# Kernel tuning notes

Hardware: AMD Instinct MI355X
Metric: run time of the kernel (lower is better)

The kernel has to match this reference:

```python
import jax, jax.numpy as jnp
import numpy as np

N_NODES = 100000
N_EDGES = 1600000
IN_FEATURES = 128
OUT_FEATURES = 32


def setup_inputs() -> dict:
    key = jax.random.key(0)
    k_x, k_w, k_r, k_c, k_v = jax.random.split(key, 5)
    x = jax.random.normal(k_x, (N_NODES, IN_FEATURES), dtype=jnp.float32)
    # One fused (in_features, out_features) weight == concat of the out_features Dense(in,1) layers
    W = jax.random.normal(k_w, (IN_FEATURES, OUT_FEATURES), dtype=jnp.float32) / np.sqrt(IN_FEATURES)
    b = jnp.zeros((OUT_FEATURES,), dtype=jnp.float32)
    edge_rows = jax.random.randint(k_r, (N_EDGES,), 0, N_NODES, dtype=jnp.int64)
    edge_cols = jax.random.randint(k_c, (N_EDGES,), 0, N_NODES, dtype=jnp.int64)
    edge_vals = jax.random.uniform(k_v, (N_EDGES,), dtype=jnp.float32)
    return {"x": x, "W": W, "b": b, "edge_rows": edge_rows,
            "edge_cols": edge_cols, "edge_vals": edge_vals}


def reference(x, W, b, edge_rows, edge_cols, edge_vals):
    # z_i = dense_i(x) for all i at once: (N, out_features)
    z = x @ W + b
    # per nonzero edge e=(r,c) with adjacency value w_e:
    #   (z*adj).values + (z^T*adj).values = w_e * (z[r] + z[c])   -> (E, out_features)
    out = edge_vals[:, None] * (z[edge_rows] + z[edge_cols])
    return out
```

## Files before the change

kernel.cpp:

```cpp
#include <hip/hip_runtime.h>

#define NODES 100000
#define IN_F 128
#define OUT_F 32

__global__ __launch_bounds__(256) void zgemm_kernel(
    const float* __restrict__ x, const float* __restrict__ W,
    const float* __restrict__ b, float* __restrict__ z, int n_nodes)
{
    __shared__ float xs[64 * IN_F];
    __shared__ float Ws[IN_F * OUT_F];
    __shared__ float bs[OUT_F];

    const int t = threadIdx.x;
    const int row0 = blockIdx.x * 64;
    const int rows = min(64, n_nodes - row0);

    {
        const float4* Wv = (const float4*)W;
        float4* Wsv = (float4*)Ws;
        #pragma unroll
        for (int i = 0; i < 4; ++i)
            Wsv[t + i * 256] = Wv[t + i * 256];
        if (t < OUT_F) bs[t] = b[t];
    }
    {
        const float4* xv = (const float4*)(x + (size_t)row0 * IN_F);
        float4* xsv = (float4*)xs;
        const int nv = rows * (IN_F / 4);
        for (int i = t; i < nv; i += 256)
            xsv[i] = xv[i];
    }
    __syncthreads();

    const int col = t & 31;
    const int rg  = t >> 5;

    float acc[8];
    #pragma unroll
    for (int i = 0; i < 8; ++i) acc[i] = 0.f;

    for (int k = 0; k < IN_F; ++k) {
        const float wv = Ws[k * OUT_F + col];
        #pragma unroll
        for (int i = 0; i < 8; ++i)
            acc[i] += xs[(rg + i * 8) * IN_F + k] * wv;
    }

    const float bb = bs[col];
    #pragma unroll
    for (int i = 0; i < 8; ++i) {
        const int r = rg + i * 8;
        if (r < rows)
            z[(size_t)(row0 + r) * OUT_F + col] = acc[i] + bb;
    }
}

__global__ __launch_bounds__(256) void edge_kernel(
    const int* __restrict__ erows, const int* __restrict__ ecols,
    const float* __restrict__ evals, const float* __restrict__ z,
    float* __restrict__ out, int n_edges)
{
    const size_t g = (size_t)blockIdx.x * 256 + threadIdx.x;
    const size_t e = g >> 3;
    if (e >= (size_t)n_edges) return;
    const int joff = (int)(g & 7) << 2;

    const int r = erows[e];
    const int c = ecols[e];
    const float w = evals[e];

    const float4 zr = *(const float4*)(z + (size_t)r * OUT_F + joff);
    const float4 zc = *(const float4*)(z + (size_t)c * OUT_F + joff);

    float4 o;
    o.x = w * (zr.x + zc.x);
    o.y = w * (zr.y + zc.y);
    o.z = w * (zr.z + zc.z);
    o.w = w * (zr.w + zc.w);

    *(float4*)(out + e * OUT_F + joff) = o;
}

extern "C" void kernel_launch(void* const* d_in, const int* in_sizes, int n_in,
                              void* d_out, int out_size, void* d_ws, size_t ws_size,
                              hipStream_t stream)
{
    const float* x  = (const float*)d_in[0];
    const float* W  = (const float*)d_in[1];
    const float* b  = (const float*)d_in[2];
    const int* erow = (const int*)d_in[3];
    const int* ecol = (const int*)d_in[4];
    const float* ev = (const float*)d_in[5];

    const int n_nodes = in_sizes[0] / IN_F;
    const int n_edges = in_sizes[3];

    float* z   = (float*)d_ws;
    float* out = (float*)d_out;

    const int gemm_blocks = (n_nodes + 63) / 64;
    zgemm_kernel<<<gemm_blocks, 256, 0, stream>>>(x, W, b, z, n_nodes);

    const size_t total_thr = (size_t)n_edges * 8;
    const int edge_blocks = (int)((total_thr + 255) / 256);
    edge_kernel<<<edge_blocks, 256, 0, stream>>>(erow, ecol, ev, z, out, n_edges);
}
```

Baseline: 326.8 us.

## Retile z GEMM to 2x4 register blocks with padded vectorized LDS reads

The node GEMM kernel now gives each thread 2 rows by 4 output columns, reading x and W from shared memory as 4-wide vectors. The x tile row stride is padded to 132 floats to avoid LDS bank conflicts on the vector reads. The aim is fewer shared-memory loads per FMA in the z = xW + b stage. The edge gather kernel is untouched and likely dominates runtime, so the overall effect is bounded by the GEMM's share.

```diff
diff --git a/kernel.cpp b/kernel.cpp
--- a/kernel.cpp
+++ b/kernel.cpp
@@ -1,14 +1,16 @@
 #include <hip/hip_runtime.h>
 
-#define NODES 100000
 #define IN_F 128
 #define OUT_F 32
+#define XS_LD 132
+
+typedef float vf4 __attribute__((ext_vector_type(4)));
 
 __global__ __launch_bounds__(256) void zgemm_kernel(
     const float* __restrict__ x, const float* __restrict__ W,
     const float* __restrict__ b, float* __restrict__ z, int n_nodes)
 {
-    __shared__ float xs[64 * IN_F];
+    __shared__ float xs[64 * XS_LD];
     __shared__ float Ws[IN_F * OUT_F];
     __shared__ float bs[OUT_F];
 
@@ -17,43 +19,52 @@
     const int rows = min(64, n_nodes - row0);
 
     {
-        const float4* Wv = (const float4*)W;
-        float4* Wsv = (float4*)Ws;
+        const vf4* Wv = (const vf4*)W;
+        vf4* Wsv = (vf4*)Ws;
         #pragma unroll
         for (int i = 0; i < 4; ++i)
             Wsv[t + i * 256] = Wv[t + i * 256];
         if (t < OUT_F) bs[t] = b[t];
     }
     {
-        const float4* xv = (const float4*)(x + (size_t)row0 * IN_F);
-        float4* xsv = (float4*)xs;
+        const vf4* xv = (const vf4*)(x + (size_t)row0 * IN_F);
         const int nv = rows * (IN_F / 4);
-        for (int i = t; i < nv; i += 256)
-            xsv[i] = xv[i];
+        for (int i = t; i < nv; i += 256) {
+            const int row = i >> 5;
+            const int kk  = i & 31;
+            *(vf4*)(xs + row * XS_LD + (kk << 2)) = xv[i];
+        }
     }
     __syncthreads();
 
-    const int col = t & 31;
-    const int rg  = t >> 5;
+    const int cg  = t & 7;
+    const int rgg = t >> 3;
+    const int c0  = cg << 2;
 
-    float acc[8];
-    #pragma unroll
-    for (int i = 0; i < 8; ++i) acc[i] = 0.f;
+    vf4 acc0 = {0.f, 0.f, 0.f, 0.f};
+    vf4 acc1 = {0.f, 0.f, 0.f, 0.f};
 
-    for (int k = 0; k < IN_F; ++k) {
-        const float wv = Ws[k * OUT_F + col];
-        #pragma unroll
-        for (int i = 0; i < 8; ++i)
-            acc[i] += xs[(rg + i * 8) * IN_F + k] * wv;
+    #pragma unroll 4
+    for (int k4 = 0; k4 < IN_F / 4; ++k4) {
+        const vf4 xa = *(const vf4*)(xs + rgg * XS_LD + (k4 << 2));
+        const vf4 xb = *(const vf4*)(xs + (rgg + 32) * XS_LD + (k4 << 2));
+        const vf4 w0 = *(const vf4*)(Ws + ((k4 << 2) + 0) * OUT_F + c0);
+        const vf4 w1 = *(const vf4*)(Ws + ((k4 << 2) + 1) * OUT_F + c0);
+        const vf4 w2 = *(const vf4*)(Ws + ((k4 << 2) + 2) * OUT_F + c0);
+        const vf4 w3 = *(const vf4*)(Ws + ((k4 << 2) + 3) * OUT_F + c0);
+
+        acc0 += xa.x * w0;  acc0 += xa.y * w1;
+        acc0 += xa.z * w2;  acc0 += xa.w * w3;
+        acc1 += xb.x * w0;  acc1 += xb.y * w1;
+        acc1 += xb.z * w2;  acc1 += xb.w * w3;
     }
 
-    const float bb = bs[col];
-    #pragma unroll
-    for (int i = 0; i < 8; ++i) {
-        const int r = rg + i * 8;
-        if (r < rows)
-            z[(size_t)(row0 + r) * OUT_F + col] = acc[i] + bb;
-    }
+    const vf4 bb = *(const vf4*)(bs + c0);
+
+    if (rgg < rows)
+        *(vf4*)(z + (size_t)(row0 + rgg) * OUT_F + c0) = acc0 + bb;
+    if (rgg + 32 < rows)
+        *(vf4*)(z + (size_t)(row0 + rgg + 32) * OUT_F + c0) = acc1 + bb;
 }
 
 __global__ __launch_bounds__(256) void edge_kernel(
```

Measured after the change: 319.9 us. 1.02x faster.
